# Kernel tuning notes

Hardware: AMD Instinct MI355X
Metric: run time of the kernel (lower is better)

The kernel has to match this reference:

```python
import jax, jax.numpy as jnp
import numpy as np

DIM = 1024
CODEBOOK_SIZE = 8192
CODEBOOK_DIM = 16
NUM_CODEBOOKS = 4
BATCH = 4
SEQ = 1024
LN_EPS = 1e-5
COS_EPS = 1e-8  # torch cosine_similarity eps


def setup_inputs() -> dict:
    key = jax.random.key(0)
    k1, k2, k3 = jax.random.split(key, 3)
    x = jax.random.normal(k1, (BATCH, SEQ, DIM), dtype=jnp.float32)
    # xavier_normal_: std = sqrt(2 / (fan_in + fan_out)) over last two dims
    xavier_std = float(np.sqrt(2.0 / (DIM + CODEBOOK_DIM)))
    rand_projs = jax.random.normal(k2, (NUM_CODEBOOKS, DIM, CODEBOOK_DIM), dtype=jnp.float32) * xavier_std
    cb = jax.random.normal(k3, (NUM_CODEBOOKS, CODEBOOK_SIZE, CODEBOOK_DIM), dtype=jnp.float32)
    cb = cb / jnp.clip(jnp.linalg.norm(cb, axis=-1, keepdims=True), 1e-12, None)  # F.normalize
    return {"x": x, "rand_projs": rand_projs, "CB": cb}


def reference(x, rand_projs, CB):
    # LayerNorm(dim, elementwise_affine=False)
    mean = jnp.mean(x, axis=-1, keepdims=True)
    var = jnp.mean(jnp.square(x - mean), axis=-1, keepdims=True)
    xn = (x - mean) * jax.lax.rsqrt(var + LN_EPS)
    # random projection: (b,t,d),(h,d,k) -> (h,b,t,k)
    proj = jnp.einsum('btd,hdk->hbtk', xn, rand_projs)
    # cosine similarity == normalize both then dot (torch clamps norm at eps)
    proj_n = proj / jnp.maximum(jnp.linalg.norm(proj, axis=-1, keepdims=True), COS_EPS)
    cb_n = CB / jnp.maximum(jnp.linalg.norm(CB, axis=-1, keepdims=True), COS_EPS)
    # distances: (h,b,t,cs)  (matches torch stack(h,b,cs,t).permute(0,1,3,2))
    distances = jnp.einsum('hbtk,hck->hbtc', proj_n, cb_n)
    # indices: argmax over codebook, stacked (h,b,t) -> permute(1,2,0) -> (b,t,h)
    indices = jnp.argmax(distances, axis=-1).transpose(1, 2, 0)
    return indices, distances
```

## Files before the change

### kernel.cpp

```cpp
#include <hip/hip_runtime.h>
#include <hip/hip_bf16.h>

#define NH 4
#define BT 4096
#define DD 1024
#define CK 16
#define CS 8192

typedef float vfloat4 __attribute__((ext_vector_type(4)));

#define WS_STATS 0
#define WS_PART  8192
#define WS_PROJN 1056768
#define WS_CBN   1318912

__global__ __launch_bounds__(256) void k_stats(const float* __restrict__ x,
                                               float* __restrict__ stats) {
  const int lane = threadIdx.x & 63;
  const int row  = blockIdx.x * 4 + (threadIdx.x >> 6);
  const float4* xr = reinterpret_cast<const float4*>(x + (size_t)row * DD);
  float4 v[4];
  float s = 0.f;
#pragma unroll
  for (int i = 0; i < 4; ++i) {
    v[i] = xr[lane + 64 * i];
    s += (v[i].x + v[i].y) + (v[i].z + v[i].w);
  }
#pragma unroll
  for (int m = 32; m >= 1; m >>= 1) s += __shfl_xor(s, m, 64);
  const float mean = s * (1.f / DD);
  float vs = 0.f;
#pragma unroll
  for (int i = 0; i < 4; ++i) {
    float a = v[i].x - mean, b = v[i].y - mean, c = v[i].z - mean, d = v[i].w - mean;
    vs += (a * a + b * b) + (c * c + d * d);
  }
#pragma unroll
  for (int m = 32; m >= 1; m >>= 1) vs += __shfl_xor(vs, m, 64);
  if (lane == 0) {
    stats[2 * row]     = mean;
    stats[2 * row + 1] = rsqrtf(vs * (1.f / DD) + 1e-5f);
  }
}

__global__ __launch_bounds__(256) void k_proj(const float* __restrict__ x,
                                              const float* __restrict__ stats,
                                              const float* __restrict__ P,
                                              float* __restrict__ part) {
  __shared__ float xa[32][68];
  __shared__ float pa[32][68];
  const int tile = blockIdx.x & 63;
  const int ds   = blockIdx.x >> 6;
  const int tid  = threadIdx.x;
  const int tx = tid & 15, ty = tid >> 4;
  const int r0 = ty * 4, o0 = tx * 4;
  float acc[4][4] = {};

  for (int dc = 0; dc < 256; dc += 32) {
    const int d0 = ds * 256 + dc;
    {
      const int row  = tid >> 2;
      const int rowg = tile * 64 + row;
      const float mean = stats[2 * rowg];
      const float rstd = stats[2 * rowg + 1];
      const float* xp = x + (size_t)rowg * DD + d0 + (tid & 3) * 8;
      float4 a = reinterpret_cast<const float4*>(xp)[0];
      float4 b = reinterpret_cast<const float4*>(xp)[1];
      const int dd = (tid & 3) * 8;
      xa[dd + 0][row] = (a.x - mean) * rstd;
      xa[dd + 1][row] = (a.y - mean) * rstd;
      xa[dd + 2][row] = (a.z - mean) * rstd;
      xa[dd + 3][row] = (a.w - mean) * rstd;
      xa[dd + 4][row] = (b.x - mean) * rstd;
      xa[dd + 5][row] = (b.y - mean) * rstd;
      xa[dd + 6][row] = (b.z - mean) * rstd;
      xa[dd + 7][row] = (b.w - mean) * rstd;
    }
    {
      const int h  = tid >> 6;
      const int f0 = (tid & 63) * 8;
      const float* pp = P + (size_t)h * DD * CK + (size_t)d0 * CK + f0;
      float4 a = reinterpret_cast<const float4*>(pp)[0];
      float4 b = reinterpret_cast<const float4*>(pp)[1];
      float vv[8] = {a.x, a.y, a.z, a.w, b.x, b.y, b.z, b.w};
#pragma unroll
      for (int j = 0; j < 8; ++j) {
        int f = f0 + j;
        pa[f >> 4][(h << 4) | (f & 15)] = vv[j];
      }
    }
    __syncthreads();
#pragma unroll
    for (int d = 0; d < 32; ++d) {
      float4 xv = *reinterpret_cast<const float4*>(&xa[d][r0]);
      float4 pv = *reinterpret_cast<const float4*>(&pa[d][o0]);
      float xr[4] = {xv.x, xv.y, xv.z, xv.w};
      float pr[4] = {pv.x, pv.y, pv.z, pv.w};
#pragma unroll
      for (int i = 0; i < 4; ++i)
#pragma unroll
        for (int j = 0; j < 4; ++j) acc[i][j] = fmaf(xr[i], pr[j], acc[i][j]);
    }
    __syncthreads();
  }
  float* pb = part + ((size_t)ds * BT + tile * 64) * 64;
#pragma unroll
  for (int i = 0; i < 4; ++i) {
    float4 o = {acc[i][0], acc[i][1], acc[i][2], acc[i][3]};
    *reinterpret_cast<float4*>(pb + (size_t)(r0 + i) * 64 + o0) = o;
  }
}

__global__ __launch_bounds__(256) void k_norm(const float* __restrict__ part,
                                              float* __restrict__ proj_n) {
  const int t   = blockIdx.x * 256 + threadIdx.x;
  const int row = t >> 2, h = t & 3;
  float s[16];
#pragma unroll
  for (int k = 0; k < 16; ++k) s[k] = 0.f;
#pragma unroll
  for (int ds = 0; ds < 4; ++ds) {
    const float* pb = part + (size_t)ds * BT * 64 + (size_t)row * 64 + h * 16;
#pragma unroll
    for (int w = 0; w < 4; ++w) {
      float4 v = reinterpret_cast<const float4*>(pb)[w];
      s[w * 4 + 0] += v.x; s[w * 4 + 1] += v.y; s[w * 4 + 2] += v.z; s[w * 4 + 3] += v.w;
    }
  }
  float nsq = 0.f;
#pragma unroll
  for (int k = 0; k < 16; ++k) nsq = fmaf(s[k], s[k], nsq);
  const float inv = 1.f / fmaxf(sqrtf(nsq), 1e-8f);
  float* op = proj_n + ((size_t)h * BT + row) * 16;
#pragma unroll
  for (int w = 0; w < 4; ++w) {
    float4 v = {s[w*4+0] * inv, s[w*4+1] * inv, s[w*4+2] * inv, s[w*4+3] * inv};
    reinterpret_cast<float4*>(op)[w] = v;
  }
}

__global__ __launch_bounds__(256) void k_cbn(const float* __restrict__ CB,
                                             float* __restrict__ cb_n) {
  const int t = blockIdx.x * 256 + threadIdx.x;
  const float4* src = reinterpret_cast<const float4*>(CB + (size_t)t * 16);
  float4 v[4];
  float nsq = 0.f;
#pragma unroll
  for (int w = 0; w < 4; ++w) {
    v[w] = src[w];
    nsq = fmaf(v[w].x, v[w].x, nsq); nsq = fmaf(v[w].y, v[w].y, nsq);
    nsq = fmaf(v[w].z, v[w].z, nsq); nsq = fmaf(v[w].w, v[w].w, nsq);
  }
  const float inv = 1.f / fmaxf(sqrtf(nsq), 1e-8f);
  float4* dst = reinterpret_cast<float4*>(cb_n + (size_t)t * 16);
#pragma unroll
  for (int w = 0; w < 4; ++w) {
    float4 o = {v[w].x * inv, v[w].y * inv, v[w].z * inv, v[w].w * inv};
    dst[w] = o;
  }
}

#define QLOADG(Q0, Q1, Q2, Q3, r)  \
  Q0 = qg[4 * (r) + 0];            \
  Q1 = qg[4 * (r) + 1];            \
  Q2 = qg[4 * (r) + 2];            \
  Q3 = qg[4 * (r) + 3];

#define ROWBODY(r, Q0, Q1, Q2, Q3)                                         \
  {                                                                        \
    float dj[4];                                                           \
    _Pragma("unroll")                                                      \
    for (int j = 0; j < 4; ++j) {                                          \
      float s =        cb[j][0].x * Q0.x;                                  \
      s = fmaf(cb[j][0].y, Q0.y, s);                                       \
      s = fmaf(cb[j][0].z, Q0.z, s);                                       \
      s = fmaf(cb[j][0].w, Q0.w, s);                                       \
      s = fmaf(cb[j][1].x, Q1.x, s);                                       \
      s = fmaf(cb[j][1].y, Q1.y, s);                                       \
      s = fmaf(cb[j][1].z, Q1.z, s);                                       \
      s = fmaf(cb[j][1].w, Q1.w, s);                                       \
      s = fmaf(cb[j][2].x, Q2.x, s);                                       \
      s = fmaf(cb[j][2].y, Q2.y, s);                                       \
      s = fmaf(cb[j][2].z, Q2.z, s);                                       \
      s = fmaf(cb[j][2].w, Q2.w, s);                                       \
      s = fmaf(cb[j][3].x, Q3.x, s);                                       \
      s = fmaf(cb[j][3].y, Q3.y, s);                                       \
      s = fmaf(cb[j][3].z, Q3.z, s);                                       \
      s = fmaf(cb[j][3].w, Q3.w, s);                                       \
      dj[j] = s;                                                           \
    }                                                                      \
    vfloat4 dots = {dj[0], dj[1], dj[2], dj[3]};                           \
    __builtin_nontemporal_store(dots,                                      \
        reinterpret_cast<vfloat4*>(db + (size_t)(r) * CS + c));            \
    _Pragma("unroll")                                                      \
    for (int j = 0; j < 4; ++j) {                                          \
      if (dj[j] > best[(r)]) { best[(r)] = dj[j]; bidx[(r)] = c + j; }     \
    }                                                                      \
  }                                                                        \
  __builtin_amdgcn_sched_barrier(0);

__global__ __launch_bounds__(256, 3) void k_dist(const float* __restrict__ proj_n,
                                                 const float* __restrict__ cb_n,
                                                 float* __restrict__ dist,
                                                 float* __restrict__ idx_out) {
  __shared__ float redv[16][4];
  __shared__ int   redi[16][4];
  const int h    = blockIdx.x >> 8;
  const int tile = blockIdx.x & 255;
  const int tid  = threadIdx.x;

  float best[16];
  int   bidx[16];
#pragma unroll
  for (int r = 0; r < 16; ++r) { best[r] = -2e30f; bidx[r] = 0; }

  const float* cbh = cb_n + (size_t)h * CS * CK;
  const float4* qg = reinterpret_cast<const float4*>(
      proj_n + ((size_t)h * BT + tile * 16) * 16);
  float* db = dist + ((size_t)h * BT + tile * 16) * CS;

  for (int cc = 0; cc < 8; ++cc) {
    const int c = cc * 1024 + tid * 4;
    float4 cb[4][4];
    const float4* cs = reinterpret_cast<const float4*>(cbh + (size_t)c * CK);
#pragma unroll
    for (int j = 0; j < 4; ++j)
#pragma unroll
      for (int w = 0; w < 4; ++w) cb[j][w] = cs[j * 4 + w];

    float4 qa0, qa1, qa2, qa3, qb0, qb1, qb2, qb3;
    QLOADG(qa0, qa1, qa2, qa3, 0)
    QLOADG(qb0, qb1, qb2, qb3, 1)  ROWBODY(0,  qa0, qa1, qa2, qa3)
    QLOADG(qa0, qa1, qa2, qa3, 2)  ROWBODY(1,  qb0, qb1, qb2, qb3)
    QLOADG(qb0, qb1, qb2, qb3, 3)  ROWBODY(2,  qa0, qa1, qa2, qa3)
    QLOADG(qa0, qa1, qa2, qa3, 4)  ROWBODY(3,  qb0, qb1, qb2, qb3)
    QLOADG(qb0, qb1, qb2, qb3, 5)  ROWBODY(4,  qa0, qa1, qa2, qa3)
    QLOADG(qa0, qa1, qa2, qa3, 6)  ROWBODY(5,  qb0, qb1, qb2, qb3)
    QLOADG(qb0, qb1, qb2, qb3, 7)  ROWBODY(6,  qa0, qa1, qa2, qa3)
    QLOADG(qa0, qa1, qa2, qa3, 8)  ROWBODY(7,  qb0, qb1, qb2, qb3)
    QLOADG(qb0, qb1, qb2, qb3, 9)  ROWBODY(8,  qa0, qa1, qa2, qa3)
    QLOADG(qa0, qa1, qa2, qa3, 10) ROWBODY(9,  qb0, qb1, qb2, qb3)
    QLOADG(qb0, qb1, qb2, qb3, 11) ROWBODY(10, qa0, qa1, qa2, qa3)
    QLOADG(qa0, qa1, qa2, qa3, 12) ROWBODY(11, qb0, qb1, qb2, qb3)
    QLOADG(qb0, qb1, qb2, qb3, 13) ROWBODY(12, qa0, qa1, qa2, qa3)
    QLOADG(qa0, qa1, qa2, qa3, 14) ROWBODY(13, qb0, qb1, qb2, qb3)
    QLOADG(qb0, qb1, qb2, qb3, 15) ROWBODY(14, qa0, qa1, qa2, qa3)
    ROWBODY(15, qb0, qb1, qb2, qb3)
  }

  const int lane = tid & 63, wv = tid >> 6;
#pragma unroll
  for (int r = 0; r < 16; ++r) {
    float v = best[r];
    int   ii = bidx[r];
#pragma unroll
    for (int m = 32; m >= 1; m >>= 1) {
      float ov = __shfl_xor(v, m, 64);
      int   oi = __shfl_xor(ii, m, 64);
      if (ov > v || (ov == v && oi < ii)) { v = ov; ii = oi; }
    }
    if (lane == 0) { redv[r][wv] = v; redi[r][wv] = ii; }
  }
  __syncthreads();
  if (tid < 16) {
    const int r = tid;
    float v = redv[r][0];
    int   ii = redi[r][0];
#pragma unroll
    for (int w = 1; w < 4; ++w) {
      float ov = redv[r][w];
      int   oi = redi[r][w];
      if (ov > v || (ov == v && oi < ii)) { v = ov; ii = oi; }
    }
    const int rowg = tile * 16 + r;
    idx_out[(size_t)rowg * 4 + h] = (float)ii;
  }
}

extern "C" void kernel_launch(void* const* d_in, const int* in_sizes, int n_in,
                              void* d_out, int out_size, void* d_ws, size_t ws_size,
                              hipStream_t stream) {
  (void)in_sizes; (void)n_in; (void)out_size; (void)ws_size;
  const float* x  = (const float*)d_in[0];
  const float* P  = (const float*)d_in[1];
  const float* CB = (const float*)d_in[2];
  float* ws  = (float*)d_ws;
  float* out = (float*)d_out;
  float* idx_out = out;
  float* dist    = out + BT * NH;

  k_stats<<<1024, 256, 0, stream>>>(x, ws + WS_STATS);
  k_proj <<<256,  256, 0, stream>>>(x, ws + WS_STATS, P, ws + WS_PART);
  k_norm <<<64,   256, 0, stream>>>(ws + WS_PART, ws + WS_PROJN);
  k_cbn  <<<128,  256, 0, stream>>>(CB, ws + WS_CBN);
  k_dist <<<1024, 256, 0, stream>>>(ws + WS_PROJN, ws + WS_CBN, dist, idx_out);
}
```

Baseline: 144.9 us.

## Split codebook across two blocks per tile and merge argmax in extra kernel

The distance kernel now splits each 16-row tile's 8192 codebook entries into two halves handled by separate blocks, doubling the grid to 2048 blocks. Each block writes a partial best value and index to workspace, and a new small kernel merges the two halves into the final index output. This is meant to improve load balance and tail utilization across the GPU's compute units. The cost is an extra kernel launch and more workspace traffic, and the partial buffers reuse the WS_PART region.

Result: no change. 147.3 us (+1.7%).

```diff
diff --git a/kernel.cpp b/kernel.cpp
--- a/kernel.cpp
+++ b/kernel.cpp
@@ -13,6 +13,8 @@
 #define WS_PART  8192
 #define WS_PROJN 1056768
 #define WS_CBN   1318912
+#define WS_PBEST WS_PART
+#define WS_PIDX  (WS_PART + 32768)
 
 __global__ __launch_bounds__(256) void k_stats(const float* __restrict__ x,
                                                float* __restrict__ stats) {
@@ -194,7 +196,7 @@
         reinterpret_cast<vfloat4*>(db + (size_t)(r) * CS + c));            \
     _Pragma("unroll")                                                      \
     for (int j = 0; j < 4; ++j) {                                          \
-      if (dj[j] > best[(r)]) { best[(r)] = dj[j]; bidx[(r)] = c + j; }     \
+      if (dj[j] > best[(r)]) { best[(r)] = dj[j]; bidx[(r)] = cg + j; }    \
     }                                                                      \
   }                                                                        \
   __builtin_amdgcn_sched_barrier(0);
@@ -202,11 +204,14 @@
 __global__ __launch_bounds__(256, 3) void k_dist(const float* __restrict__ proj_n,
                                                  const float* __restrict__ cb_n,
                                                  float* __restrict__ dist,
-                                                 float* __restrict__ idx_out) {
+                                                 float* __restrict__ pbest,
+                                                 int* __restrict__ pidx) {
   __shared__ float redv[16][4];
   __shared__ int   redi[16][4];
-  const int h    = blockIdx.x >> 8;
-  const int tile = blockIdx.x & 255;
+  const int h    = blockIdx.x >> 9;
+  const int rest = blockIdx.x & 511;
+  const int tile = rest >> 1;
+  const int half = rest & 1;
   const int tid  = threadIdx.x;
 
   float best[16];
@@ -214,13 +219,14 @@
 #pragma unroll
   for (int r = 0; r < 16; ++r) { best[r] = -2e30f; bidx[r] = 0; }
 
-  const float* cbh = cb_n + (size_t)h * CS * CK;
+  const float* cbh = cb_n + (size_t)h * CS * CK + (size_t)half * 4096 * CK;
   const float4* qg = reinterpret_cast<const float4*>(
       proj_n + ((size_t)h * BT + tile * 16) * 16);
-  float* db = dist + ((size_t)h * BT + tile * 16) * CS;
-
-  for (int cc = 0; cc < 8; ++cc) {
-    const int c = cc * 1024 + tid * 4;
+  float* db = dist + ((size_t)h * BT + tile * 16) * CS + half * 4096;
+
+  for (int cc = 0; cc < 4; ++cc) {
+    const int c  = cc * 1024 + tid * 4;
+    const int cg = half * 4096 + c;
     float4 cb[4][4];
     const float4* cs = reinterpret_cast<const float4*>(cbh + (size_t)c * CK);
 #pragma unroll
@@ -272,9 +278,25 @@
       int   oi = redi[r][w];
       if (ov > v || (ov == v && oi < ii)) { v = ov; ii = oi; }
     }
-    const int rowg = tile * 16 + r;
-    idx_out[(size_t)rowg * 4 + h] = (float)ii;
-  }
+    const int slot = (((h * 256 + tile) * 2) + half) * 16 + r;
+    pbest[slot] = v;
+    pidx[slot]  = ii;
+  }
+}
+
+__global__ __launch_bounds__(256) void k_amax(const float* __restrict__ pbest,
+                                              const int* __restrict__ pidx,
+                                              float* __restrict__ idx_out) {
+  const int t   = blockIdx.x * 256 + threadIdx.x;
+  const int h   = t >> 12;
+  const int row = t & 4095;
+  const int tile = row >> 4, r = row & 15;
+  const int s0 = (((h * 256 + tile) * 2) + 0) * 16 + r;
+  const int s1 = s0 + 16;
+  const float b0 = pbest[s0], b1 = pbest[s1];
+  const int   i0 = pidx[s0],  i1 = pidx[s1];
+  const int win = (b1 > b0) ? i1 : i0;
+  idx_out[(size_t)row * 4 + h] = (float)win;
 }
 
 extern "C" void kernel_launch(void* const* d_in, const int* in_sizes, int n_in,
@@ -293,5 +315,7 @@
   k_proj <<<256,  256, 0, stream>>>(x, ws + WS_STATS, P, ws + WS_PART);
   k_norm <<<64,   256, 0, stream>>>(ws + WS_PART, ws + WS_PROJN);
   k_cbn  <<<128,  256, 0, stream>>>(CB, ws + WS_CBN);
-  k_dist <<<1024, 256, 0, stream>>>(ws + WS_PROJN, ws + WS_CBN, dist, idx_out);
-}
+  k_dist <<<2048, 256, 0, stream>>>(ws + WS_PROJN, ws + WS_CBN, dist,
+                                    ws + WS_PBEST, (int*)(ws + WS_PIDX));
+  k_amax <<<64,   256, 0, stream>>>(ws + WS_PBEST, (int*)(ws + WS_PIDX), idx_out);
+}
```
